# Performance work log

Hardware: AMD Instinct MI355X
Metric: run time of the kernel (lower is better)

The kernel has to match this reference:

```python
import jax, jax.numpy as jnp
import numpy as np

NC = 64
B, H, W = 32, 128, 128


def setup_inputs() -> dict:
    key = jax.random.key(0)
    kx, = jax.random.split(key, 1)
    x = jax.random.normal(kx, (B, NC, H, W), dtype=jnp.float32)
    # params as initialized in the torch module
    exp_param = jnp.eye(NC, dtype=jnp.float32)[:, :, None, None]  # (nc, nc, 1, 1)
    bias = jnp.zeros((NC, 1, 1), dtype=jnp.float32)               # (nc, 1, 1)
    return {"x": x, "exp_param": exp_param, "bias": bias}


def reference(x, exp_param, bias):
    # x: (B, nc, H, W); exp_param: (nc, nc, 1, 1); bias: (nc, 1, 1)
    xr = jax.nn.relu(x) + 0.1  # strictly positive -> log is safe
    # prod_i xr[b,i,h,w] ** E[i,j]  ==  exp( sum_i E[i,j] * log xr[b,i,h,w] )
    # Fused form avoids materializing the (B, nc, nc, H, W) intermediate.
    E = exp_param[:, :, 0, 0]  # (nc_in=i, nc_out=j)
    logx = jnp.log(xr)
    out = jnp.exp(jnp.einsum('bihw,ij->bjhw', logx, E)) + bias  # (B, nc, H, W)
    return out
```

## Files before the change

### kernel.cpp

```cpp
#include <hip/hip_runtime.h>

#define NCH 64
#define HWSZ 16384
#define NPOINTS (32 * HWSZ)
#define NTILES (NPOINTS / 64)

typedef __attribute__((ext_vector_type(8))) short bf16x8;
typedef __attribute__((ext_vector_type(4))) float f32x4;

union fragU { bf16x8 v; unsigned int u[4]; };

static __device__ __forceinline__ unsigned int fbits(float f) {
    return __float_as_uint(f);
}
static __device__ __forceinline__ float bf16_up_bits(unsigned int b) {
    return __uint_as_float(b & 0xFFFF0000u);
}

__global__ __launch_bounds__(256, 2) void fused_log_einsum_exp(
    const float* __restrict__ x,
    const float* __restrict__ E,
    const float* __restrict__ bias,
    float* __restrict__ out)
{
    const int lane = threadIdx.x & 63;
    const int wv   = threadIdx.x >> 6;
    const int lg   = lane >> 4;
    const int ln   = lane & 15;

    const int p0 = blockIdx.x * 64 + wv * 16;
    const size_t base = (size_t)(p0 & ~(HWSZ - 1)) * NCH
                      + (size_t)(p0 & (HWSZ - 1)) + ln;

    float xr[16];
    #pragma unroll
    for (int e = 0; e < 16; ++e)
        xr[e] = x[base + (size_t)((e >> 3) * 32 + lg * 8 + (e & 7)) * HWSZ];

    bf16x8 ah[4][2];
    #pragma unroll
    for (int m = 0; m < 4; ++m) {
        #pragma unroll
        for (int kk = 0; kk < 2; ++kk) {
            fragU h;
            #pragma unroll
            for (int w = 0; w < 4; ++w) {
                const int i0 = kk * 32 + lg * 8 + 2 * w;
                const int j  = m * 16 + ln;
                h.u[w] = (fbits(E[(i0 + 1) * NCH + j]) & 0xFFFF0000u)
                       | (fbits(E[i0 * NCH + j]) >> 16);
            }
            ah[m][kk] = h.v;
        }
    }

    float bv[4][4];
    #pragma unroll
    for (int m = 0; m < 4; ++m)
        #pragma unroll
        for (int r = 0; r < 4; ++r)
            bv[m][r] = bias[m * 16 + lg * 4 + r];

    bf16x8 bh[2], bl[2];
    #pragma unroll
    for (int kk = 0; kk < 2; ++kk) {
        fragU h_, l_;
        #pragma unroll
        for (int w = 0; w < 4; ++w) {
            const float lx0 = __logf(fmaxf(xr[kk * 8 + 2 * w],     0.0f) + 0.1f);
            const float lx1 = __logf(fmaxf(xr[kk * 8 + 2 * w + 1], 0.0f) + 0.1f);
            h_.u[w] = (fbits(lx1) & 0xFFFF0000u) | (fbits(lx0) >> 16);
            const float lo0 = lx0 - bf16_up_bits(fbits(lx0));
            const float lo1 = lx1 - bf16_up_bits(fbits(lx1));
            l_.u[w] = (fbits(lo1) & 0xFFFF0000u) | (fbits(lo0) >> 16);
        }
        bh[kk] = h_.v; bl[kk] = l_.v;
    }

    #pragma unroll
    for (int m = 0; m < 4; ++m) {
        f32x4 acc = {0.f, 0.f, 0.f, 0.f};
        #pragma unroll
        for (int kk = 0; kk < 2; ++kk) {
            acc = __builtin_amdgcn_mfma_f32_16x16x32_bf16(ah[m][kk], bh[kk], acc, 0, 0, 0);
            acc = __builtin_amdgcn_mfma_f32_16x16x32_bf16(ah[m][kk], bl[kk], acc, 0, 0, 0);
        }
        #pragma unroll
        for (int r = 0; r < 4; ++r) {
            const int j = m * 16 + lg * 4 + r;
            __builtin_nontemporal_store(__expf(acc[r]) + bv[m][r],
                                        &out[base + (size_t)j * HWSZ]);
        }
    }
}

extern "C" void kernel_launch(void* const* d_in, const int* in_sizes, int n_in,
                              void* d_out, int out_size, void* d_ws, size_t ws_size,
                              hipStream_t stream) {
    const float* x    = (const float*)d_in[0];
    const float* E    = (const float*)d_in[1];
    const float* bias = (const float*)d_in[2];
    float* out = (float*)d_out;

    dim3 grid(NTILES), block(256);
    hipLaunchKernelGGL(fused_log_einsum_exp, grid, block, 0, stream,
                       x, E, bias, out);
}
```

Measured before the change: 256.8 us.

## Stage input tiles through LDS with double-buffered async loads in persistent blocks

Switches to a persistent grid of 1024 blocks, each handling 4 tiles of 128 points. Input tiles are loaded via global_load_lds into a double-buffered, XOR-swizzled LDS array so the next tile's load overlaps the current tile's log/MFMA/exp work. Operand roles are swapped so outputs come out as contiguous float4 stores instead of scalar nontemporal stores. This aims to hide memory latency and improve coalescing, but adds barriers, hand-written vmcnt waits and 64KB of LDS per block, which may limit occupancy.

```diff
diff --git a/kernel.cpp b/kernel.cpp
--- a/kernel.cpp
+++ b/kernel.cpp
@@ -3,7 +3,10 @@
 #define NCH 64
 #define HWSZ 16384
 #define NPOINTS (32 * HWSZ)
-#define NTILES (NPOINTS / 64)
+#define TPTS 128
+#define NTILES (NPOINTS / TPTS)
+#define NBLOCKS 1024
+#define TPB 4
 
 typedef __attribute__((ext_vector_type(8))) short bf16x8;
 typedef __attribute__((ext_vector_type(4))) float f32x4;
@@ -13,7 +16,7 @@
 static __device__ __forceinline__ unsigned int fbits(float f) {
     return __float_as_uint(f);
 }
-static __device__ __forceinline__ float bf16_up_bits(unsigned int b) {
+static __device__ __forceinline__ float bfup(unsigned int b) {
     return __uint_as_float(b & 0xFFFF0000u);
 }
 
@@ -23,21 +26,14 @@
     const float* __restrict__ bias,
     float* __restrict__ out)
 {
+    __shared__ float lx[2][NCH][TPTS];
+
     const int lane = threadIdx.x & 63;
     const int wv   = threadIdx.x >> 6;
     const int lg   = lane >> 4;
     const int ln   = lane & 15;
 
-    const int p0 = blockIdx.x * 64 + wv * 16;
-    const size_t base = (size_t)(p0 & ~(HWSZ - 1)) * NCH
-                      + (size_t)(p0 & (HWSZ - 1)) + ln;
-
-    float xr[16];
-    #pragma unroll
-    for (int e = 0; e < 16; ++e)
-        xr[e] = x[base + (size_t)((e >> 3) * 32 + lg * 8 + (e & 7)) * HWSZ];
-
-    bf16x8 ah[4][2];
+    bf16x8 bE[4][2];
     #pragma unroll
     for (int m = 0; m < 4; ++m) {
         #pragma unroll
@@ -50,48 +46,98 @@
                 h.u[w] = (fbits(E[(i0 + 1) * NCH + j]) & 0xFFFF0000u)
                        | (fbits(E[i0 * NCH + j]) >> 16);
             }
-            ah[m][kk] = h.v;
+            bE[m][kk] = h.v;
         }
     }
 
-    float bv[4][4];
+    float bj[4];
     #pragma unroll
-    for (int m = 0; m < 4; ++m)
-        #pragma unroll
-        for (int r = 0; r < 4; ++r)
-            bv[m][r] = bias[m * 16 + lg * 4 + r];
+    for (int m = 0; m < 4; ++m) bj[m] = bias[m * 16 + ln];
 
-    bf16x8 bh[2], bl[2];
+#define TILE_PB(T) ((size_t)(((T) * TPTS) & ~(HWSZ - 1)) * NCH \
+                  + (size_t)(((T) * TPTS) & (HWSZ - 1)))
+
+#define STAGE(BSEL, T) do {                                                    \
+    const size_t pb_ = TILE_PB(T);                                             \
+    _Pragma("unroll")                                                          \
+    for (int n_ = 0; n_ < 8; ++n_) {                                           \
+        const int row_   = wv * 16 + 2 * n_;                                   \
+        const int plane_ = row_ + (lane >> 5);                                 \
+        const int sw_    = ((plane_ >> 3) & 1) << 4;                           \
+        const size_t g_  = pb_ + (size_t)plane_ * HWSZ                         \
+                         + (size_t)(((lane & 31) * 4) ^ sw_);                  \
+        __builtin_amdgcn_global_load_lds(                                      \
+            (const __attribute__((address_space(1))) unsigned int*)(x + g_),   \
+            (__attribute__((address_space(3))) unsigned int*)&lx[BSEL][row_][0],\
+            16, 0, 0);                                                         \
+    }                                                                          \
+} while (0)
+
+#define COMPUTE(BSEL, T) do {                                                  \
+    const size_t po_ = TILE_PB(T);                                             \
+    _Pragma("unroll")                                                          \
+    for (int sub_ = 0; sub_ < 2; ++sub_) {                                     \
+        const int pt_ = wv * 32 + sub_ * 16 + ln;                              \
+        fragU ah_[2], al_[2];                                                  \
+        _Pragma("unroll")                                                      \
+        for (int kk_ = 0; kk_ < 2; ++kk_) {                                    \
+            _Pragma("unroll")                                                  \
+            for (int w_ = 0; w_ < 4; ++w_) {                                   \
+                const int i0_ = kk_ * 32 + lg * 8 + 2 * w_;                    \
+                const float v0_ = lx[BSEL][i0_][pt_ ^ (((i0_ >> 3) & 1) << 4)];\
+                const float v1_ = lx[BSEL][i0_ + 1]                            \
+                                    [pt_ ^ ((((i0_ + 1) >> 3) & 1) << 4)];     \
+                const float a0_ = __logf(fmaxf(v0_, 0.0f) + 0.1f);             \
+                const float a1_ = __logf(fmaxf(v1_, 0.0f) + 0.1f);             \
+                ah_[kk_].u[w_] = (fbits(a1_) & 0xFFFF0000u) | (fbits(a0_) >> 16); \
+                const float b0_ = a0_ - bfup(fbits(a0_));                      \
+                const float b1_ = a1_ - bfup(fbits(a1_));                      \
+                al_[kk_].u[w_] = (fbits(b1_) & 0xFFFF0000u) | (fbits(b0_) >> 16); \
+            }                                                                  \
+        }                                                                      \
+        _Pragma("unroll")                                                      \
+        for (int m_ = 0; m_ < 4; ++m_) {                                       \
+            f32x4 acc_ = {0.f, 0.f, 0.f, 0.f};                                 \
+            _Pragma("unroll")                                                  \
+            for (int kk_ = 0; kk_ < 2; ++kk_) {                                \
+                acc_ = __builtin_amdgcn_mfma_f32_16x16x32_bf16(                \
+                           ah_[kk_].v, bE[m_][kk_], acc_, 0, 0, 0);            \
+                acc_ = __builtin_amdgcn_mfma_f32_16x16x32_bf16(                \
+                           al_[kk_].v, bE[m_][kk_], acc_, 0, 0, 0);            \
+            }                                                                  \
+            float4 o_;                                                         \
+            o_.x = __expf(acc_[0]) + bj[m_];                                   \
+            o_.y = __expf(acc_[1]) + bj[m_];                                   \
+            o_.z = __expf(acc_[2]) + bj[m_];                                   \
+            o_.w = __expf(acc_[3]) + bj[m_];                                   \
+            *reinterpret_cast<float4*>(out + po_                               \
+                + (size_t)(m_ * 16 + ln) * HWSZ                                \
+                + (size_t)(wv * 32 + sub_ * 16 + lg * 4)) = o_;                \
+        }                                                                      \
+    }                                                                          \
+} while (0)
+
+    STAGE(0, (int)blockIdx.x);
     #pragma unroll
-    for (int kk = 0; kk < 2; ++kk) {
-        fragU h_, l_;
-        #pragma unroll
-        for (int w = 0; w < 4; ++w) {
-            const float lx0 = __logf(fmaxf(xr[kk * 8 + 2 * w],     0.0f) + 0.1f);
-            const float lx1 = __logf(fmaxf(xr[kk * 8 + 2 * w + 1], 0.0f) + 0.1f);
-            h_.u[w] = (fbits(lx1) & 0xFFFF0000u) | (fbits(lx0) >> 16);
-            const float lo0 = lx0 - bf16_up_bits(fbits(lx0));
-            const float lo1 = lx1 - bf16_up_bits(fbits(lx1));
-            l_.u[w] = (fbits(lo1) & 0xFFFF0000u) | (fbits(lo0) >> 16);
+    for (int t = 0; t < TPB; ++t) {
+        if (t + 1 < TPB) STAGE((t + 1) & 1, (int)blockIdx.x + (t + 1) * NBLOCKS);
+        if (t == 0 || t == TPB - 1) {
+            asm volatile("s_waitcnt vmcnt(8)" ::: "memory");
+        } else {
+            asm volatile("s_waitcnt vmcnt(16)" ::: "memory");
         }
-        bh[kk] = h_.v; bl[kk] = l_.v;
+        __builtin_amdgcn_s_barrier();
+        __builtin_amdgcn_sched_barrier(0);
+        COMPUTE(t & 1, (int)blockIdx.x + t * NBLOCKS);
+        if (t + 1 < TPB) {
+            __builtin_amdgcn_s_barrier();
+            __builtin_amdgcn_sched_barrier(0);
+        }
     }
 
-    #pragma unroll
-    for (int m = 0; m < 4; ++m) {
-        f32x4 acc = {0.f, 0.f, 0.f, 0.f};
-        #pragma unroll
-        for (int kk = 0; kk < 2; ++kk) {
-            acc = __builtin_amdgcn_mfma_f32_16x16x32_bf16(ah[m][kk], bh[kk], acc, 0, 0, 0);
-            acc = __builtin_amdgcn_mfma_f32_16x16x32_bf16(ah[m][kk], bl[kk], acc, 0, 0, 0);
-        }
-        #pragma unroll
-        for (int r = 0; r < 4; ++r) {
-            const int j = m * 16 + lg * 4 + r;
-            __builtin_nontemporal_store(__expf(acc[r]) + bv[m][r],
-                                        &out[base + (size_t)j * HWSZ]);
-        }
-    }
+#undef TILE_PB
+#undef STAGE
+#undef COMPUTE
 }
 
 extern "C" void kernel_launch(void* const* d_in, const int* in_sizes, int n_in,
@@ -102,7 +148,7 @@
     const float* bias = (const float*)d_in[2];
     float* out = (float*)d_out;
 
-    dim3 grid(NTILES), block(256);
+    dim3 grid(NBLOCKS), block(256);
     hipLaunchKernelGGL(fused_log_einsum_exp, grid, block, 0, stream,
                        x, E, bias, out);
 }
```

Result: faster. 242.6 us (-5.5%).
